# Optimization experiments

Hardware: AMD Instinct MI355X
Metric: run time of the kernel (lower is better)

The kernel has to match this reference:

```python
import jax, jax.numpy as jnp
import numpy as np

N, E, ND, ED, HID, H, L = 50000, 800000, 32, 16, 96, 4, 3
C = HID // H  # per-head channels = 24
NEG_SLOPE = 0.2
LN_EPS = 1e-5


def setup_inputs() -> dict:
    key = jax.random.key(0)
    ks = iter(jax.random.split(key, 40))
    def r(shape, s=0.05):
        return jax.random.normal(next(ks), shape, jnp.float32) * s
    return dict(
        x=r((N, ND), 1.0),
        edge_index=jax.random.randint(next(ks), (2, E), 0, N),
        edge_attr=r((E, ED), 1.0),
        proj_w=r((ND, HID)), proj_b=jnp.zeros((HID,), jnp.float32),
        lin_l_w=r((L, HID, HID)), lin_l_b=jnp.zeros((L, HID), jnp.float32),
        lin_r_w=r((L, HID, HID)), lin_r_b=jnp.zeros((L, HID), jnp.float32),
        lin_e_w=r((L, ED, HID)),
        att=r((L, H, C)),
        conv_b=jnp.zeros((L, HID), jnp.float32),
        ln_g=jnp.ones((L, HID), jnp.float32), ln_b=jnp.zeros((L, HID), jnp.float32),
        head_w1=r((HID, HID // 2)), head_b1=jnp.zeros((HID // 2,), jnp.float32),
        head_w2=r((HID // 2, 1)), head_b2=jnp.zeros((1,), jnp.float32),
    )


def _layernorm(h, g, b):
    mu = h.mean(-1, keepdims=True)
    var = ((h - mu) ** 2).mean(-1, keepdims=True)
    return (h - mu) / jnp.sqrt(var + LN_EPS) * g + b


def _gatv2(x, src, dst, edge_attr, Wl, bl, Wr, br, We, att, bias):
    # GATv2Conv (PyG semantics, eval mode): x_l = lin_l(x) for source, x_r = lin_r(x) for target
    xl = (x @ Wl + bl).reshape(N, H, C)
    xr = (x @ Wr + br).reshape(N, H, C)
    e = (edge_attr @ We).reshape(E, H, C)
    m = jax.nn.leaky_relu(xl[src] + xr[dst] + e, NEG_SLOPE)  # [E,H,C]
    alpha = (m * att).sum(-1)  # [E,H]
    # segment softmax over incoming edges of each target node
    amax = jax.ops.segment_max(alpha, dst, num_segments=N)  # [N,H]
    ea = jnp.exp(alpha - amax[dst])
    denom = jax.ops.segment_sum(ea, dst, num_segments=N)
    alpha = ea / (denom[dst] + 1e-16)
    out = jax.ops.segment_sum(xl[src] * alpha[..., None], dst, num_segments=N)
    return out.reshape(N, HID) + bias


def reference(x, edge_index, edge_attr, proj_w, proj_b, lin_l_w, lin_l_b, lin_r_w,
              lin_r_b, lin_e_w, att, conv_b, ln_g, ln_b, head_w1, head_b1, head_w2, head_b2):
    src, dst = edge_index[0], edge_index[1]
    h = x @ proj_w + proj_b
    for l in range(L):
        m = _gatv2(h, src, dst, edge_attr, lin_l_w[l], lin_l_b[l], lin_r_w[l],
                   lin_r_b[l], lin_e_w[l], att[l], conv_b[l])
        h = _layernorm(h + m, ln_g[l], ln_b[l])
    h = jax.nn.gelu(h @ head_w1 + head_b1, approximate=False)
    return (h @ head_w2 + head_b2).squeeze(-1)
```

## Files before the change

kernel.cpp:

```cpp
#include <hip/hip_runtime.h>

constexpr int N_NODES = 50000;
constexpr int N_EDGES = 800000;
constexpr int ND  = 32;
constexpr int ED  = 16;
constexpr int HID = 96;
constexpr int NLAYER = 3;

typedef unsigned short ushort_t;
typedef unsigned int uint_t;
typedef __attribute__((ext_vector_type(8))) short bf16x8;
typedef __attribute__((ext_vector_type(4))) float f32x4;

__device__ __forceinline__ float bf2f(ushort_t u) {
    union { float f; uint_t ui; } c; c.ui = ((uint_t)u) << 16; return c.f;
}
__device__ __forceinline__ ushort_t f2bf(float f) {
    uint_t u = __float_as_uint(f);
    return (ushort_t)((u + 0x7FFFu + ((u >> 16) & 1u)) >> 16);
}

__global__ void k_count_deg(const int* __restrict__ dst, int* __restrict__ deg) {
    int e4 = blockIdx.x * 256 + threadIdx.x;
    if (e4 * 4 >= N_EDGES) return;
    int4 d = ((const int4*)dst)[e4];
    atomicAdd(&deg[d.x], 1); atomicAdd(&deg[d.y], 1);
    atomicAdd(&deg[d.z], 1); atomicAdd(&deg[d.w], 1);
}

__global__ void k_scan_block(const int* __restrict__ deg, int* __restrict__ rowptr,
                             int* __restrict__ bsum) {
    __shared__ int s[256];
    int i = blockIdx.x * 256 + threadIdx.x;
    int v = (i < N_NODES) ? deg[i] : 0;
    s[threadIdx.x] = v;
    __syncthreads();
    for (int off = 1; off < 256; off <<= 1) {
        int t = (threadIdx.x >= off) ? s[threadIdx.x - off] : 0;
        __syncthreads();
        s[threadIdx.x] += t;
        __syncthreads();
    }
    if (i < N_NODES) rowptr[i] = s[threadIdx.x] - v;
    if (threadIdx.x == 255) bsum[blockIdx.x] = s[255];
}

__global__ void k_scan_bsum(int* __restrict__ bsum, int nb) {
    __shared__ int s[256];
    int t = threadIdx.x;
    int v = (t < nb) ? bsum[t] : 0;
    s[t] = v;
    __syncthreads();
    for (int off = 1; off < 256; off <<= 1) {
        int tv = (t >= off) ? s[t - off] : 0;
        __syncthreads();
        s[t] += tv;
        __syncthreads();
    }
    if (t < nb) bsum[t] = s[t] - v;
}

__global__ void k_scan_add(int* __restrict__ rowptr, const int* __restrict__ bsum,
                           int* __restrict__ fill) {
    int i = blockIdx.x * 256 + threadIdx.x;
    if (i < N_NODES) {
        int v = rowptr[i] + bsum[blockIdx.x];
        rowptr[i] = v;
        fill[i] = v;
    }
    if (i == 0) rowptr[N_NODES] = N_EDGES;
}

__global__ void k_scatter(const int* __restrict__ src, const int* __restrict__ dst,
                          const float* __restrict__ eattr, int* __restrict__ fill,
                          int* __restrict__ srcs, int* __restrict__ pdst,
                          ushort_t* __restrict__ ea) {
    int e4 = blockIdx.x * 256 + threadIdx.x;
    if (e4 * 4 >= N_EDGES) return;
    int4 s = ((const int4*)src)[e4];
    int4 d = ((const int4*)dst)[e4];
    int e0 = e4 * 4;
    int sv[4] = {s.x, s.y, s.z, s.w};
    int dv[4] = {d.x, d.y, d.z, d.w};
#pragma unroll
    for (int j = 0; j < 4; j++) {
        int pos = atomicAdd(&fill[dv[j]], 1);
        srcs[pos] = sv[j];
        pdst[pos] = dv[j];
        const float4* er = (const float4*)(eattr + (size_t)(e0 + j) * ED);
        uint2* ew = (uint2*)(ea + (size_t)pos * ED);
#pragma unroll
        for (int q = 0; q < 4; q++) {
            float4 v = er[q];
            uint_t lo = (uint_t)f2bf(v.x) | ((uint_t)f2bf(v.y) << 16);
            uint_t hi = (uint_t)f2bf(v.z) | ((uint_t)f2bf(v.w) << 16);
            ew[q] = make_uint2(lo, hi);
        }
    }
}

__global__ __launch_bounds__(192) void k_proj(const float* __restrict__ x,
                                              const float* __restrict__ pw,
                                              const float* __restrict__ pb,
                                              float* __restrict__ h) {
    int t = threadIdx.x;
    int c = t % 96, half = t / 96;
    float wreg[ND];
#pragma unroll
    for (int k = 0; k < ND; k++) wreg[k] = pw[k * HID + c];
    float b = pb[c];
    int n0 = blockIdx.x * 16 + half * 8;
    for (int i = 0; i < 8; i += 2) {
        int na = n0 + i, nb = na + 1;
        const float4* xa = (const float4*)(x + (size_t)na * ND);
        const float4* xb = (const float4*)(x + (size_t)nb * ND);
        float accA = b, accB = b;
#pragma unroll
        for (int k4 = 0; k4 < ND / 4; k4++) {
            float4 va = xa[k4], vb = xb[k4];
            accA += va.x * wreg[4 * k4] + va.y * wreg[4 * k4 + 1] +
                    va.z * wreg[4 * k4 + 2] + va.w * wreg[4 * k4 + 3];
            accB += vb.x * wreg[4 * k4] + vb.y * wreg[4 * k4 + 1] +
                    vb.z * wreg[4 * k4 + 2] + vb.w * wreg[4 * k4 + 3];
        }
        h[(size_t)na * HID + c] = accA;
        h[(size_t)nb * HID + c] = accB;
    }
}

__global__ __launch_bounds__(256) void k_linlr_mfma(
    const float* __restrict__ h, const float* __restrict__ Wl,
    const float* __restrict__ bl, const float* __restrict__ Wr,
    const float* __restrict__ br, ushort_t* __restrict__ xl,
    ushort_t* __restrict__ xr) {
    __shared__ ushort_t sW[192 * 104];
    __shared__ float sB[192];
    int t = threadIdx.x;

    for (int idx = t; idx < 192 * 96; idx += 256) {
        int n = idx % 192, k = idx / 192;
        float v = (n < 96) ? Wl[k * 96 + n] : Wr[k * 96 + (n - 96)];
        sW[n * 104 + k] = f2bf(v);
    }
    if (t < 192) sB[t] = (t < 96) ? bl[t] : br[t - 96];
    __syncthreads();

    int wv = t >> 6, lane = t & 63;
    int m0 = blockIdx.x * 64 + wv * 16;
    if (m0 >= N_NODES) return;
    int m = lane & 15, quad = lane >> 4;

    bf16x8 afr[3];
    const float* hrow = h + (size_t)(m0 + m) * HID;
#pragma unroll
    for (int s = 0; s < 3; s++) {
        float4 v0 = *(const float4*)(hrow + s * 32 + quad * 8);
        float4 v1 = *(const float4*)(hrow + s * 32 + quad * 8 + 4);
        bf16x8 a;
        a[0] = (short)f2bf(v0.x); a[1] = (short)f2bf(v0.y);
        a[2] = (short)f2bf(v0.z); a[3] = (short)f2bf(v0.w);
        a[4] = (short)f2bf(v1.x); a[5] = (short)f2bf(v1.y);
        a[6] = (short)f2bf(v1.z); a[7] = (short)f2bf(v1.w);
        afr[s] = a;
    }

#pragma unroll
    for (int nt = 0; nt < 12; nt++) {
        int ch = nt * 16 + m;
        f32x4 acc = {0.f, 0.f, 0.f, 0.f};
#pragma unroll
        for (int s = 0; s < 3; s++) {
            bf16x8 bfr = *(const bf16x8*)(sW + (nt * 16 + m) * 104 + s * 32 + quad * 8);
            acc = __builtin_amdgcn_mfma_f32_16x16x32_bf16(afr[s], bfr, acc, 0, 0, 0);
        }
        float bias = sB[ch];
        ushort_t* dst = (ch < 96) ? (xl + (size_t)(m0 + quad * 4) * HID + ch)
                                  : (xr + (size_t)(m0 + quad * 4) * HID + (ch - 96));
#pragma unroll
        for (int r = 0; r < 4; r++)
            dst[(size_t)r * HID] = f2bf(acc[r] + bias);
    }
}

__global__ __launch_bounds__(256) void k_ev(
    const ushort_t* __restrict__ xlb, const ushort_t* __restrict__ xrb,
    const ushort_t* __restrict__ ea, const int* __restrict__ srcs,
    const int* __restrict__ pdst, const float* __restrict__ WeL,
    const float* __restrict__ attL, float4* __restrict__ ev) {
    int wid = blockIdx.x * 4 + (threadIdx.x >> 6);
    int lane = threadIdx.x & 63;
    if (wid >= N_EDGES / 128) return;
    int col = lane & 15, quad = lane >> 4;
    int comp = col & 1, base = col >> 1;

    int2 sp = *(const int2*)(srcs + wid * 128 + 2 * lane);
    int2 dp = *(const int2*)(pdst + wid * 128 + 2 * lane);

    bf16x8 afr[6];
#pragma unroll
    for (int mc = 0; mc < 6; mc++) {
        bf16x8 a = {0, 0, 0, 0, 0, 0, 0, 0};
        if (quad < 2) {
#pragma unroll
            for (int j = 0; j < 8; j++)
                a[j] = (short)f2bf(WeL[(quad * 8 + j) * HID + mc * 16 + col]);
        }
        afr[mc] = a;
    }
    float attr[6][4];
#pragma unroll
    for (int mc = 0; mc < 6; mc++)
#pragma unroll
        for (int r = 0; r < 4; r++)
            attr[mc][r] = attL[mc * 16 + quad * 4 + r];

    bf16x8 bfr[2];
    uint2 xu[2][6], ru[2][6];

    auto getsd = [&](int b, int& sv, int& dv) {
        int sl = b * 8 + base;
        int sx = __shfl(sp.x, sl), sy = __shfl(sp.y, sl);
        int dx = __shfl(dp.x, sl), dy = __shfl(dp.y, sl);
        sv = comp ? sy : sx;
        dv = comp ? dy : dx;
    };
    auto issue = [&](int b, int pp) {
        int sv, dv;
        getsd(b, sv, dv);
        int p = wid * 128 + b * 16 + col;
        bf16x8 z8 = {0, 0, 0, 0, 0, 0, 0, 0};
        bfr[pp] = (quad < 2) ? *(const bf16x8*)(ea + (size_t)p * ED + quad * 8) : z8;
        const ushort_t* xp = xlb + (size_t)sv * HID + quad * 4;
        const ushort_t* rp = xrb + (size_t)dv * HID + quad * 4;
#pragma unroll
        for (int mc = 0; mc < 6; mc++) {
            xu[pp][mc] = *(const uint2*)(xp + mc * 16);
            ru[pp][mc] = *(const uint2*)(rp + mc * 16);
        }
    };

    issue(0, 0);
#pragma unroll
    for (int b = 0; b < 8; b++) {
        int pp = b & 1;
        if (b < 7) issue(b + 1, pp ^ 1);

        f32x4 zero4 = {0.f, 0.f, 0.f, 0.f};
        f32x4 d[6];
#pragma unroll
        for (int mc = 0; mc < 6; mc++)
            d[mc] = __builtin_amdgcn_mfma_f32_16x16x32_bf16(afr[mc], bfr[pp], zero4, 0, 0, 0);

        float s[6];
#pragma unroll
        for (int mc = 0; mc < 6; mc++) {
            uint2 a = xu[pp][mc], r = ru[pp][mc];
            float x0 = bf2f((ushort_t)(a.x & 0xffff)), x1 = bf2f((ushort_t)(a.x >> 16));
            float x2 = bf2f((ushort_t)(a.y & 0xffff)), x3 = bf2f((ushort_t)(a.y >> 16));
            float r0 = bf2f((ushort_t)(r.x & 0xffff)), r1 = bf2f((ushort_t)(r.x >> 16));
            float r2 = bf2f((ushort_t)(r.y & 0xffff)), r3 = bf2f((ushort_t)(r.y >> 16));
            float z0 = x0 + r0 + d[mc][0]; z0 = z0 > 0.f ? z0 : 0.2f * z0;
            float z1 = x1 + r1 + d[mc][1]; z1 = z1 > 0.f ? z1 : 0.2f * z1;
            float z2 = x2 + r2 + d[mc][2]; z2 = z2 > 0.f ? z2 : 0.2f * z2;
            float z3 = x3 + r3 + d[mc][3]; z3 = z3 > 0.f ? z3 : 0.2f * z3;
            s[mc] = z0 * attr[mc][0] + z1 * attr[mc][1] +
                    z2 * attr[mc][2] + z3 * attr[mc][3];
        }
        float U[6], V[6];
#pragma unroll
        for (int mc = 0; mc < 6; mc++) {
            U[mc] = s[mc] + __shfl_xor(s[mc], 16);
            V[mc] = U[mc] + __shfl_xor(U[mc], 32);
        }
        if (quad == 0) {
            float h0 = V[0] + U[1];
            float h1 = (V[1] - U[1]) + V[2];
            float h2 = V[3] + U[4];
            float h3 = (V[4] - U[4]) + V[5];
            int p = wid * 128 + b * 16 + col;
            ev[p] = make_float4(__expf(h0), __expf(h1), __expf(h2), __expf(h3));
        }
    }
}

__global__ __launch_bounds__(256) void k_agg(
    const ushort_t* __restrict__ xlb, const float* __restrict__ evf,
    const int* __restrict__ srcs, const int* __restrict__ rowptr,
    const float* __restrict__ convb, const float* __restrict__ lng,
    const float* __restrict__ lnb, float* __restrict__ h) {
    int lane = threadIdx.x & 63;
    int node = blockIdx.x * 4 + (threadIdx.x >> 6);
    int slot = lane >> 4, q = lane & 15;
    int c0 = q * 6, head = q >> 2;
    int beg = rowptr[node], end = rowptr[node + 1];
    int cnt = (end - beg + 3) >> 2;

    float n0 = 0.f, n1 = 0.f, n2 = 0.f, n3 = 0.f, n4 = 0.f, n5 = 0.f, den = 0.f;
    if (cnt > 0) {
        int p = beg + slot;
        bool v = p < end;
        int pc = v ? p : beg;
        int src = srcs[pc];
        float evv = evf[4 * pc + head];
        const ushort_t* xp = xlb + (size_t)src * HID + c0;
        uint_t a0 = *(const uint_t*)(xp);
        uint_t a1 = *(const uint_t*)(xp + 2);
        uint_t a2 = *(const uint_t*)(xp + 4);
        for (int it = 0; it < cnt; ++it) {
            int pn = beg + (it + 1) * 4 + slot;
            bool vn = pn < end;
            int pcn = vn ? pn : beg;
            int srcn = srcs[pcn];
            float evn = evf[4 * pcn + head];
            const ushort_t* xpn = xlb + (size_t)srcn * HID + c0;
            uint_t b0 = *(const uint_t*)(xpn);
            uint_t b1 = *(const uint_t*)(xpn + 2);
            uint_t b2 = *(const uint_t*)(xpn + 4);

            float e = v ? evv : 0.f;
            n0 += e * bf2f((ushort_t)(a0 & 0xffff));
            n1 += e * bf2f((ushort_t)(a0 >> 16));
            n2 += e * bf2f((ushort_t)(a1 & 0xffff));
            n3 += e * bf2f((ushort_t)(a1 >> 16));
            n4 += e * bf2f((ushort_t)(a2 & 0xffff));
            n5 += e * bf2f((ushort_t)(a2 >> 16));
            den += e;

            v = vn; evv = evn; a0 = b0; a1 = b1; a2 = b2;
        }
    }
    n0 += __shfl_xor(n0, 16); n0 += __shfl_xor(n0, 32);
    n1 += __shfl_xor(n1, 16); n1 += __shfl_xor(n1, 32);
    n2 += __shfl_xor(n2, 16); n2 += __shfl_xor(n2, 32);
    n3 += __shfl_xor(n3, 16); n3 += __shfl_xor(n3, 32);
    n4 += __shfl_xor(n4, 16); n4 += __shfl_xor(n4, 32);
    n5 += __shfl_xor(n5, 16); n5 += __shfl_xor(n5, 32);
    den += __shfl_xor(den, 16); den += __shfl_xor(den, 32);

    size_t nb = (size_t)node * HID + c0;
    float inv = 1.f / (den + 1e-16f);
    float v0 = h[nb + 0] + n0 * inv + convb[c0 + 0];
    float v1 = h[nb + 1] + n1 * inv + convb[c0 + 1];
    float v2 = h[nb + 2] + n2 * inv + convb[c0 + 2];
    float v3 = h[nb + 3] + n3 * inv + convb[c0 + 3];
    float v4 = h[nb + 4] + n4 * inv + convb[c0 + 4];
    float v5 = h[nb + 5] + n5 * inv + convb[c0 + 5];
    float sm = v0 + v1 + v2 + v3 + v4 + v5;
    sm += __shfl_xor(sm, 1); sm += __shfl_xor(sm, 2);
    sm += __shfl_xor(sm, 4); sm += __shfl_xor(sm, 8);
    float mu = sm * (1.f / 96.f);
    float d0 = v0 - mu, d1 = v1 - mu, d2 = v2 - mu;
    float d3 = v3 - mu, d4 = v4 - mu, d5 = v5 - mu;
    float sv = d0 * d0 + d1 * d1 + d2 * d2 + d3 * d3 + d4 * d4 + d5 * d5;
    sv += __shfl_xor(sv, 1); sv += __shfl_xor(sv, 2);
    sv += __shfl_xor(sv, 4); sv += __shfl_xor(sv, 8);
    float rstd = rsqrtf(sv * (1.f / 96.f) + 1e-5f);
    if (slot == 0) {
        h[nb + 0] = d0 * rstd * lng[c0 + 0] + lnb[c0 + 0];
        h[nb + 1] = d1 * rstd * lng[c0 + 1] + lnb[c0 + 1];
        h[nb + 2] = d2 * rstd * lng[c0 + 2] + lnb[c0 + 2];
        h[nb + 3] = d3 * rstd * lng[c0 + 3] + lnb[c0 + 3];
        h[nb + 4] = d4 * rstd * lng[c0 + 4] + lnb[c0 + 4];
        h[nb + 5] = d5 * rstd * lng[c0 + 5] + lnb[c0 + 5];
    }
}

__global__ __launch_bounds__(256) void k_head_mfma(
    const float* __restrict__ h, const float* __restrict__ W1,
    const float* __restrict__ b1, const float* __restrict__ W2,
    const float* __restrict__ b2, float* __restrict__ out) {
    __shared__ ushort_t sW[48 * 104];
    __shared__ float sB1[48];
    __shared__ float sW2[48];
    int t = threadIdx.x;
    for (int idx = t; idx < 48 * 96; idx += 256) {
        int j = idx % 48, k = idx / 48;
        sW[j * 104 + k] = f2bf(W1[k * 48 + j]);
    }
    if (t < 48) { sB1[t] = b1[t]; sW2[t] = W2[t]; }
    __syncthreads();

    int wv = t >> 6, lane = t & 63;
    int m0 = blockIdx.x * 64 + wv * 16;
    if (m0 >= N_NODES) return;
    int col = lane & 15, quad = lane >> 4;

    bf16x8 afr[3];
    const float* hrow = h + (size_t)(m0 + col) * HID;
#pragma unroll
    for (int s = 0; s < 3; s++) {
        float4 v0 = *(const float4*)(hrow + s * 32 + quad * 8);
        float4 v1 = *(const float4*)(hrow + s * 32 + quad * 8 + 4);
        bf16x8 a;
        a[0] = (short)f2bf(v0.x); a[1] = (short)f2bf(v0.y);
        a[2] = (short)f2bf(v0.z); a[3] = (short)f2bf(v0.w);
        a[4] = (short)f2bf(v1.x); a[5] = (short)f2bf(v1.y);
        a[6] = (short)f2bf(v1.z); a[7] = (short)f2bf(v1.w);
        afr[s] = a;
    }

    const float inv_sqrt2 = 0.70710678118654752f;
    float y0 = 0.f, y1 = 0.f, y2 = 0.f, y3 = 0.f;
#pragma unroll
    for (int nt = 0; nt < 3; nt++) {
        f32x4 acc = {0.f, 0.f, 0.f, 0.f};
#pragma unroll
        for (int s = 0; s < 3; s++) {
            bf16x8 bfr = *(const bf16x8*)(sW + (nt * 16 + col) * 104 + s * 32 + quad * 8);
            acc = __builtin_amdgcn_mfma_f32_16x16x32_bf16(afr[s], bfr, acc, 0, 0, 0);
        }
        int ch = nt * 16 + col;
        float bias = sB1[ch], w2 = sW2[ch];
        float v, g;
        v = acc[0] + bias; g = 0.5f * v * (1.f + erff(v * inv_sqrt2)); y0 += g * w2;
        v = acc[1] + bias; g = 0.5f * v * (1.f + erff(v * inv_sqrt2)); y1 += g * w2;
        v = acc[2] + bias; g = 0.5f * v * (1.f + erff(v * inv_sqrt2)); y2 += g * w2;
        v = acc[3] + bias; g = 0.5f * v * (1.f + erff(v * inv_sqrt2)); y3 += g * w2;
    }
    y0 += __shfl_xor(y0, 1); y0 += __shfl_xor(y0, 2);
    y0 += __shfl_xor(y0, 4); y0 += __shfl_xor(y0, 8);
    y1 += __shfl_xor(y1, 1); y1 += __shfl_xor(y1, 2);
    y1 += __shfl_xor(y1, 4); y1 += __shfl_xor(y1, 8);
    y2 += __shfl_xor(y2, 1); y2 += __shfl_xor(y2, 2);
    y2 += __shfl_xor(y2, 4); y2 += __shfl_xor(y2, 8);
    y3 += __shfl_xor(y3, 1); y3 += __shfl_xor(y3, 2);
    y3 += __shfl_xor(y3, 4); y3 += __shfl_xor(y3, 8);
    if (col == 0) {
        float bb = b2[0];
        out[m0 + quad * 4 + 0] = y0 + bb;
        out[m0 + quad * 4 + 1] = y1 + bb;
        out[m0 + quad * 4 + 2] = y2 + bb;
        out[m0 + quad * 4 + 3] = y3 + bb;
    }
}

extern "C" void kernel_launch(void* const* d_in, const int* in_sizes, int n_in,
                              void* d_out, int out_size, void* d_ws, size_t ws_size,
                              hipStream_t stream) {
    const float* x       = (const float*)d_in[0];
    const int*   eidx    = (const int*)  d_in[1];
    const float* eattr   = (const float*)d_in[2];
    const float* proj_w  = (const float*)d_in[3];
    const float* proj_b  = (const float*)d_in[4];
    const float* lin_l_w = (const float*)d_in[5];
    const float* lin_l_b = (const float*)d_in[6];
    const float* lin_r_w = (const float*)d_in[7];
    const float* lin_r_b = (const float*)d_in[8];
    const float* lin_e_w = (const float*)d_in[9];
    const float* att     = (const float*)d_in[10];
    const float* conv_b  = (const float*)d_in[11];
    const float* ln_g    = (const float*)d_in[12];
    const float* ln_b    = (const float*)d_in[13];
    const float* head_w1 = (const float*)d_in[14];
    const float* head_b1 = (const float*)d_in[15];
    const float* head_w2 = (const float*)d_in[16];
    const float* head_b2 = (const float*)d_in[17];
    float* out = (float*)d_out;

    char* p = (char*)d_ws;
    auto alloc = [&](size_t bytes) -> char* {
        char* r = p;
        p += (bytes + 255) & ~size_t(255);
        return r;
    };
    float*    h      = (float*)alloc(sizeof(float) * (size_t)N_NODES * HID);
    ushort_t* xl     = (ushort_t*)alloc(2 * (size_t)N_NODES * HID);
    ushort_t* xr     = (ushort_t*)alloc(2 * (size_t)N_NODES * HID);
    int*      deg    = (int*)alloc(4 * (size_t)N_NODES);
    int*      fill   = (int*)alloc(4 * (size_t)N_NODES);
    int*      rowptr = (int*)alloc(4 * (size_t)(N_NODES + 1));
    int*      bsum   = (int*)alloc(4 * 256);
    int*      srcs   = (int*)alloc(4 * ((size_t)N_EDGES + 256));
    int*      pdst   = (int*)alloc(4 * ((size_t)N_EDGES + 256));
    ushort_t* ea_csr = (ushort_t*)alloc(2 * (size_t)N_EDGES * ED);
    float4*   ev     = (float4*)alloc(16 * (size_t)N_EDGES);

    const int* srcA = eidx;
    const int* dstA = eidx + N_EDGES;

    int ebl4 = (N_EDGES / 4 + 255) / 256;
    int nbl  = (N_NODES + 255) / 256;

    hipMemsetAsync(deg, 0, 4 * (size_t)N_NODES, stream);
    k_count_deg<<<ebl4, 256, 0, stream>>>(dstA, deg);
    k_scan_block<<<nbl, 256, 0, stream>>>(deg, rowptr, bsum);
    k_scan_bsum<<<1, 256, 0, stream>>>(bsum, nbl);
    k_scan_add<<<nbl, 256, 0, stream>>>(rowptr, bsum, fill);
    k_scatter<<<ebl4, 256, 0, stream>>>(srcA, dstA, eattr, fill, srcs, pdst, ea_csr);

    k_proj<<<N_NODES / 16, 192, 0, stream>>>(x, proj_w, proj_b, h);
    for (int l = 0; l < NLAYER; l++) {
        k_linlr_mfma<<<(N_NODES + 63) / 64, 256, 0, stream>>>(
            h, lin_l_w + (size_t)l * HID * HID, lin_l_b + (size_t)l * HID,
            lin_r_w + (size_t)l * HID * HID, lin_r_b + (size_t)l * HID, xl, xr);
        k_ev<<<1563, 256, 0, stream>>>(xl, xr, ea_csr, srcs, pdst,
                                       lin_e_w + (size_t)l * ED * HID,
                                       att + (size_t)l * HID,
                                       (float4*)ev);
        k_agg<<<N_NODES / 4, 256, 0, stream>>>(
            xl, (const float*)ev, srcs, rowptr, conv_b + (size_t)l * HID,
            ln_g + (size_t)l * HID, ln_b + (size_t)l * HID, h);
    }
    k_head_mfma<<<(N_NODES + 63) / 64, 256, 0, stream>>>(h, head_w1, head_b1,
                                                         head_w2, head_b2, out);
}
```

Before: 587.2 us.

## Compute edge scores in original order and store edge ids in CSR

The scatter no longer permutes edge attributes into CSR order. It writes packed (src, edge id) pairs, and a separate coalesced kernel converts edge_attr to bf16 in place. k_ev now processes edges in their original order, so its ea reads are sequential, but its xr[dst] gathers become random instead of clustered by destination. k_agg reads the score through the edge id, which turns the ev load into an indirect gather.

```diff
diff --git a/kernel.cpp b/kernel.cpp
--- a/kernel.cpp
+++ b/kernel.cpp
@@ -72,9 +72,7 @@
 }
 
 __global__ void k_scatter(const int* __restrict__ src, const int* __restrict__ dst,
-                          const float* __restrict__ eattr, int* __restrict__ fill,
-                          int* __restrict__ srcs, int* __restrict__ pdst,
-                          ushort_t* __restrict__ ea) {
+                          int* __restrict__ fill, int2* __restrict__ csre) {
     int e4 = blockIdx.x * 256 + threadIdx.x;
     if (e4 * 4 >= N_EDGES) return;
     int4 s = ((const int4*)src)[e4];
@@ -85,18 +83,21 @@
 #pragma unroll
     for (int j = 0; j < 4; j++) {
         int pos = atomicAdd(&fill[dv[j]], 1);
-        srcs[pos] = sv[j];
-        pdst[pos] = dv[j];
-        const float4* er = (const float4*)(eattr + (size_t)(e0 + j) * ED);
-        uint2* ew = (uint2*)(ea + (size_t)pos * ED);
-#pragma unroll
-        for (int q = 0; q < 4; q++) {
-            float4 v = er[q];
-            uint_t lo = (uint_t)f2bf(v.x) | ((uint_t)f2bf(v.y) << 16);
-            uint_t hi = (uint_t)f2bf(v.z) | ((uint_t)f2bf(v.w) << 16);
-            ew[q] = make_uint2(lo, hi);
-        }
-    }
+        csre[pos] = make_int2(sv[j], e0 + j);
+    }
+}
+
+__global__ void k_cvt(const float* __restrict__ eattr, ushort_t* __restrict__ ea) {
+    int tid = blockIdx.x * 256 + threadIdx.x;
+    size_t base = (size_t)tid * 8;
+    float4 v0 = *(const float4*)(eattr + base);
+    float4 v1 = *(const float4*)(eattr + base + 4);
+    uint4 w;
+    w.x = (uint_t)f2bf(v0.x) | ((uint_t)f2bf(v0.y) << 16);
+    w.y = (uint_t)f2bf(v0.z) | ((uint_t)f2bf(v0.w) << 16);
+    w.z = (uint_t)f2bf(v1.x) | ((uint_t)f2bf(v1.y) << 16);
+    w.w = (uint_t)f2bf(v1.z) | ((uint_t)f2bf(v1.w) << 16);
+    *(uint4*)(ea + base) = w;
 }
 
 __global__ __launch_bounds__(192) void k_proj(const float* __restrict__ x,
@@ -184,8 +185,8 @@
 
 __global__ __launch_bounds__(256) void k_ev(
     const ushort_t* __restrict__ xlb, const ushort_t* __restrict__ xrb,
-    const ushort_t* __restrict__ ea, const int* __restrict__ srcs,
-    const int* __restrict__ pdst, const float* __restrict__ WeL,
+    const ushort_t* __restrict__ ea, const int* __restrict__ srcE,
+    const int* __restrict__ dstE, const float* __restrict__ WeL,
     const float* __restrict__ attL, float4* __restrict__ ev) {
     int wid = blockIdx.x * 4 + (threadIdx.x >> 6);
     int lane = threadIdx.x & 63;
@@ -193,8 +194,8 @@
     int col = lane & 15, quad = lane >> 4;
     int comp = col & 1, base = col >> 1;
 
-    int2 sp = *(const int2*)(srcs + wid * 128 + 2 * lane);
-    int2 dp = *(const int2*)(pdst + wid * 128 + 2 * lane);
+    int2 sp = *(const int2*)(srcE + wid * 128 + 2 * lane);
+    int2 dp = *(const int2*)(dstE + wid * 128 + 2 * lane);
 
     bf16x8 afr[6];
 #pragma unroll
@@ -285,7 +286,7 @@
 
 __global__ __launch_bounds__(256) void k_agg(
     const ushort_t* __restrict__ xlb, const float* __restrict__ evf,
-    const int* __restrict__ srcs, const int* __restrict__ rowptr,
+    const int2* __restrict__ csre, const int* __restrict__ rowptr,
     const float* __restrict__ convb, const float* __restrict__ lng,
     const float* __restrict__ lnb, float* __restrict__ h) {
     int lane = threadIdx.x & 63;
@@ -300,9 +301,9 @@
         int p = beg + slot;
         bool v = p < end;
         int pc = v ? p : beg;
-        int src = srcs[pc];
-        float evv = evf[4 * pc + head];
-        const ushort_t* xp = xlb + (size_t)src * HID + c0;
+        int2 se = csre[pc];
+        float evv = evf[4 * se.y + head];
+        const ushort_t* xp = xlb + (size_t)se.x * HID + c0;
         uint_t a0 = *(const uint_t*)(xp);
         uint_t a1 = *(const uint_t*)(xp + 2);
         uint_t a2 = *(const uint_t*)(xp + 4);
@@ -310,9 +311,9 @@
             int pn = beg + (it + 1) * 4 + slot;
             bool vn = pn < end;
             int pcn = vn ? pn : beg;
-            int srcn = srcs[pcn];
-            float evn = evf[4 * pcn + head];
-            const ushort_t* xpn = xlb + (size_t)srcn * HID + c0;
+            int2 sen = csre[pcn];
+            float evn = evf[4 * sen.y + head];
+            const ushort_t* xpn = xlb + (size_t)sen.x * HID + c0;
             uint_t b0 = *(const uint_t*)(xpn);
             uint_t b1 = *(const uint_t*)(xpn + 2);
             uint_t b2 = *(const uint_t*)(xpn + 4);
@@ -470,9 +471,8 @@
     int*      fill   = (int*)alloc(4 * (size_t)N_NODES);
     int*      rowptr = (int*)alloc(4 * (size_t)(N_NODES + 1));
     int*      bsum   = (int*)alloc(4 * 256);
-    int*      srcs   = (int*)alloc(4 * ((size_t)N_EDGES + 256));
-    int*      pdst   = (int*)alloc(4 * ((size_t)N_EDGES + 256));
-    ushort_t* ea_csr = (ushort_t*)alloc(2 * (size_t)N_EDGES * ED);
+    int2*     csre   = (int2*)alloc(8 * (size_t)N_EDGES);
+    ushort_t* ea_bf  = (ushort_t*)alloc(2 * (size_t)N_EDGES * ED);
     float4*   ev     = (float4*)alloc(16 * (size_t)N_EDGES);
 
     const int* srcA = eidx;
@@ -486,19 +486,20 @@
     k_scan_block<<<nbl, 256, 0, stream>>>(deg, rowptr, bsum);
     k_scan_bsum<<<1, 256, 0, stream>>>(bsum, nbl);
     k_scan_add<<<nbl, 256, 0, stream>>>(rowptr, bsum, fill);
-    k_scatter<<<ebl4, 256, 0, stream>>>(srcA, dstA, eattr, fill, srcs, pdst, ea_csr);
+    k_scatter<<<ebl4, 256, 0, stream>>>(srcA, dstA, fill, csre);
+    k_cvt<<<N_EDGES * ED / 8 / 256, 256, 0, stream>>>(eattr, ea_bf);
 
     k_proj<<<N_NODES / 16, 192, 0, stream>>>(x, proj_w, proj_b, h);
     for (int l = 0; l < NLAYER; l++) {
         k_linlr_mfma<<<(N_NODES + 63) / 64, 256, 0, stream>>>(
             h, lin_l_w + (size_t)l * HID * HID, lin_l_b + (size_t)l * HID,
             lin_r_w + (size_t)l * HID * HID, lin_r_b + (size_t)l * HID, xl, xr);
-        k_ev<<<1563, 256, 0, stream>>>(xl, xr, ea_csr, srcs, pdst,
+        k_ev<<<1563, 256, 0, stream>>>(xl, xr, ea_bf, srcA, dstA,
                                        lin_e_w + (size_t)l * ED * HID,
                                        att + (size_t)l * HID,
                                        (float4*)ev);
         k_agg<<<N_NODES / 4, 256, 0, stream>>>(
-            xl, (const float*)ev, srcs, rowptr, conv_b + (size_t)l * HID,
+            xl, (const float*)ev, csre, rowptr, conv_b + (size_t)l * HID,
             ln_g + (size_t)l * HID, ln_b + (size_t)l * HID, h);
     }
     k_head_mfma<<<(N_NODES + 63) / 64, 256, 0, stream>>>(h, head_w1, head_b1,
```

Result: slower. 650.5 us (+10.8%).

## Split CSR build into index scatter plus coalesced edge-attribute gather

Applied to the files above, without the earlier changes.

The CSR build previously scattered each edge's source, destination and bf16-converted attributes to random positions in one kernel. Now a thin scatter kernel writes only an (src, edge id) pair per CSR slot. A second kernel walks CSR order, gathers the attributes by edge id and writes them contiguously, turning scattered writes into scattered reads. The degree-count and scatter kernels also move from four edges per thread to one, at the cost of an extra launch and an 8-byte-per-edge intermediate buffer.

```diff
diff --git a/kernel.cpp b/kernel.cpp
--- a/kernel.cpp
+++ b/kernel.cpp
@@ -21,11 +21,8 @@
 }
 
 __global__ void k_count_deg(const int* __restrict__ dst, int* __restrict__ deg) {
-    int e4 = blockIdx.x * 256 + threadIdx.x;
-    if (e4 * 4 >= N_EDGES) return;
-    int4 d = ((const int4*)dst)[e4];
-    atomicAdd(&deg[d.x], 1); atomicAdd(&deg[d.y], 1);
-    atomicAdd(&deg[d.z], 1); atomicAdd(&deg[d.w], 1);
+    int e = blockIdx.x * 256 + threadIdx.x;
+    if (e < N_EDGES) atomicAdd(&deg[dst[e]], 1);
 }
 
 __global__ void k_scan_block(const int* __restrict__ deg, int* __restrict__ rowptr,
@@ -72,31 +69,37 @@
 }
 
 __global__ void k_scatter(const int* __restrict__ src, const int* __restrict__ dst,
-                          const float* __restrict__ eattr, int* __restrict__ fill,
-                          int* __restrict__ srcs, int* __restrict__ pdst,
-                          ushort_t* __restrict__ ea) {
-    int e4 = blockIdx.x * 256 + threadIdx.x;
-    if (e4 * 4 >= N_EDGES) return;
-    int4 s = ((const int4*)src)[e4];
-    int4 d = ((const int4*)dst)[e4];
-    int e0 = e4 * 4;
-    int sv[4] = {s.x, s.y, s.z, s.w};
-    int dv[4] = {d.x, d.y, d.z, d.w};
-#pragma unroll
-    for (int j = 0; j < 4; j++) {
-        int pos = atomicAdd(&fill[dv[j]], 1);
-        srcs[pos] = sv[j];
-        pdst[pos] = dv[j];
-        const float4* er = (const float4*)(eattr + (size_t)(e0 + j) * ED);
-        uint2* ew = (uint2*)(ea + (size_t)pos * ED);
-#pragma unroll
-        for (int q = 0; q < 4; q++) {
-            float4 v = er[q];
-            uint_t lo = (uint_t)f2bf(v.x) | ((uint_t)f2bf(v.y) << 16);
-            uint_t hi = (uint_t)f2bf(v.z) | ((uint_t)f2bf(v.w) << 16);
-            ew[q] = make_uint2(lo, hi);
-        }
-    }
+                          int* __restrict__ fill, int2* __restrict__ csre) {
+    int e = blockIdx.x * 256 + threadIdx.x;
+    if (e >= N_EDGES) return;
+    int d = dst[e];
+    int pos = atomicAdd(&fill[d], 1);
+    csre[pos] = make_int2(src[e], e);
+}
+
+__global__ void k_gather(const int2* __restrict__ csre, const int* __restrict__ dstA,
+                         const float* __restrict__ eattr, int* __restrict__ srcs,
+                         int* __restrict__ pdst, ushort_t* __restrict__ ea) {
+    int p = blockIdx.x * 256 + threadIdx.x;
+    if (p >= N_EDGES) return;
+    int2 se = csre[p];
+    int e = se.y;
+    srcs[p] = se.x;
+    pdst[p] = dstA[e];
+    const float4* er = (const float4*)(eattr + (size_t)e * ED);
+    float4 v0 = er[0], v1 = er[1], v2 = er[2], v3 = er[3];
+    uint4 w0, w1;
+    w0.x = (uint_t)f2bf(v0.x) | ((uint_t)f2bf(v0.y) << 16);
+    w0.y = (uint_t)f2bf(v0.z) | ((uint_t)f2bf(v0.w) << 16);
+    w0.z = (uint_t)f2bf(v1.x) | ((uint_t)f2bf(v1.y) << 16);
+    w0.w = (uint_t)f2bf(v1.z) | ((uint_t)f2bf(v1.w) << 16);
+    w1.x = (uint_t)f2bf(v2.x) | ((uint_t)f2bf(v2.y) << 16);
+    w1.y = (uint_t)f2bf(v2.z) | ((uint_t)f2bf(v2.w) << 16);
+    w1.z = (uint_t)f2bf(v3.x) | ((uint_t)f2bf(v3.y) << 16);
+    w1.w = (uint_t)f2bf(v3.z) | ((uint_t)f2bf(v3.w) << 16);
+    uint4* ew = (uint4*)(ea + (size_t)p * ED);
+    ew[0] = w0;
+    ew[1] = w1;
 }
 
 __global__ __launch_bounds__(192) void k_proj(const float* __restrict__ x,
@@ -470,6 +473,7 @@
     int*      fill   = (int*)alloc(4 * (size_t)N_NODES);
     int*      rowptr = (int*)alloc(4 * (size_t)(N_NODES + 1));
     int*      bsum   = (int*)alloc(4 * 256);
+    int2*     csre   = (int2*)alloc(8 * (size_t)N_EDGES);
     int*      srcs   = (int*)alloc(4 * ((size_t)N_EDGES + 256));
     int*      pdst   = (int*)alloc(4 * ((size_t)N_EDGES + 256));
     ushort_t* ea_csr = (ushort_t*)alloc(2 * (size_t)N_EDGES * ED);
@@ -478,15 +482,16 @@
     const int* srcA = eidx;
     const int* dstA = eidx + N_EDGES;
 
-    int ebl4 = (N_EDGES / 4 + 255) / 256;
-    int nbl  = (N_NODES + 255) / 256;
+    int ebl = (N_EDGES + 255) / 256;
+    int nbl = (N_NODES + 255) / 256;
 
     hipMemsetAsync(deg, 0, 4 * (size_t)N_NODES, stream);
-    k_count_deg<<<ebl4, 256, 0, stream>>>(dstA, deg);
+    k_count_deg<<<ebl, 256, 0, stream>>>(dstA, deg);
     k_scan_block<<<nbl, 256, 0, stream>>>(deg, rowptr, bsum);
     k_scan_bsum<<<1, 256, 0, stream>>>(bsum, nbl);
     k_scan_add<<<nbl, 256, 0, stream>>>(rowptr, bsum, fill);
-    k_scatter<<<ebl4, 256, 0, stream>>>(srcA, dstA, eattr, fill, srcs, pdst, ea_csr);
+    k_scatter<<<ebl, 256, 0, stream>>>(srcA, dstA, fill, csre);
+    k_gather<<<ebl, 256, 0, stream>>>(csre, dstA, eattr, srcs, pdst, ea_csr);
 
     k_proj<<<N_NODES / 16, 192, 0, stream>>>(x, proj_w, proj_b, h);
     for (int l = 0; l < NLAYER; l++) {
```

Result: no change. 592.8 us (+1.0%).
